# Kernel optimization log

Hardware: AMD Instinct MI355X
Metric: run time of the kernel (lower is better)

Reference implementation:

```python
import jax, jax.numpy as jnp
import numpy as np

EPS = 1e-8

def _cosine(a, b):
    # a: (b,h,s,d), b: (b,1,1,d) -> (b,h,s). torch eps semantics: clamp each norm.
    num = jnp.sum(a * b, axis=-1)
    na = jnp.maximum(jnp.linalg.norm(a, axis=-1), EPS)
    nb = jnp.maximum(jnp.linalg.norm(b, axis=-1), EPS)
    return num / (na * nb)

def setup_inputs() -> dict:
    B, H, S, DH, DM = 2, 16, 2048, 64, 1024
    key = jax.random.key(0)
    ks = jax.random.split(key, 8)
    queries = jax.random.normal(ks[0], (B, H, S, DH), dtype=jnp.float32)
    keys = jax.random.normal(ks[1], (B, H, S, DH), dtype=jnp.float32)
    context = jax.random.normal(ks[2], (B, DM), dtype=jnp.float32)
    prev_state = jax.random.normal(ks[3], (B, S, DH), dtype=jnp.float32)
    # causal mask (1 = keep, 0 = masked), shape (B,1,S,S)
    attention_mask = jnp.broadcast_to(jnp.tril(jnp.ones((S, S), dtype=jnp.int32)), (B, 1, S, S))
    # learned params (Linear weights stored torch-style as (out, in))
    cfm_ctx_w = jax.random.normal(ks[4], (DH, DM), dtype=jnp.float32) / np.sqrt(DM)
    cfm_state_w = jax.random.normal(ks[5], (DH, DH), dtype=jnp.float32) / np.sqrt(DH)
    afm_ctx_w = jax.random.normal(ks[6], (DH, DM), dtype=jnp.float32) / np.sqrt(DM)
    cfm_scale = jnp.full((1,), 0.1, dtype=jnp.float32)
    afm_scale = jnp.full((1,), 0.1, dtype=jnp.float32)
    alpha = jnp.asarray(0.1, dtype=jnp.float32)
    beta = jnp.asarray(0.1, dtype=jnp.float32)
    return dict(queries=queries, keys=keys, context=context, prev_state=prev_state,
                attention_mask=attention_mask, cfm_ctx_w=cfm_ctx_w, cfm_state_w=cfm_state_w,
                cfm_scale=cfm_scale, afm_ctx_w=afm_ctx_w, afm_scale=afm_scale,
                alpha=alpha, beta=beta)

def reference(queries, keys, context, prev_state, attention_mask,
              cfm_ctx_w, cfm_state_w, cfm_scale, afm_ctx_w, afm_scale, alpha, beta):
    B, H, S, DH = queries.shape
    # QK^T / sqrt(d_k): (b,h,s,s)
    attn_scores = jnp.einsum('bhqd,bhkd->bhqk', queries, keys) / jnp.sqrt(jnp.asarray(DH, queries.dtype))
    # ---- CFM ----
    cfm_ctx = (context @ cfm_ctx_w.T)[:, None, None, :]            # (b,1,1,dh)
    witt = _cosine(keys, cfm_ctx)                                   # (b,h,s)
    state = (prev_state @ cfm_state_w.T)[:, None, :, :]             # (b,1,s,dh)
    hamming = jnp.mean(((keys > 0) != (state > 0)).astype(keys.dtype), axis=-1)  # (b,h,s)
    cfm = ((witt + (1.0 - hamming)) * cfm_scale[0])[:, :, None, :]  # (b,h,1,s)
    # ---- AFM (no key_probs -> uniform entropy 1/S) ----
    afm_ctx = (context @ afm_ctx_w.T)[:, None, None, :]
    contradiction = jax.nn.relu(-_cosine(keys, afm_ctx))            # (b,h,s)
    entropy = jnp.full_like(contradiction, 1.0 / S)
    afm = ((contradiction + entropy) * afm_scale[0])[:, :, None, :]
    composite = attn_scores + alpha * cfm - beta * afm
    composite = jnp.where(attention_mask == 0, -jnp.inf, composite)
    return composite
```

## Files before the change

### kernel.cpp

```cpp
#include <hip/hip_runtime.h>
#include <math.h>

#define BB 2
#define HH 16
#define SS 2048
#define DHD 64
#define DMD 1024
#define EPSF 1e-8f
#define NEG_FILL -1.0e30f

typedef __attribute__((ext_vector_type(8))) short bf16x8;
typedef __attribute__((ext_vector_type(4))) float f32x4;

#define WS_BIAS_F   1024
#define WS_CONV_F   66560
#define CONV_ELEMS  (BB * HH * SS * DHD)
#define GRAN_TOTAL  (CONV_ELEMS / 8)
#define WS_NEEDED_B ((size_t)WS_CONV_F * 4 + (size_t)CONV_ELEMS * 2 * 4)

static __device__ __forceinline__ unsigned short f2bf(float f) {
    unsigned u = __float_as_uint(f);
    u += 0x7FFFu + ((u >> 16) & 1u);
    return (unsigned short)(u >> 16);
}
static __device__ __forceinline__ float bf2f(unsigned short h) {
    return __uint_as_float(((unsigned)h) << 16);
}
static __device__ __forceinline__ void cvt8(const float* p, bf16x8& h8, bf16x8& l8) {
    float4 v0 = *(const float4*)p;
    float4 v1 = *(const float4*)(p + 4);
    float vf[8] = {v0.x, v0.y, v0.z, v0.w, v1.x, v1.y, v1.z, v1.w};
    #pragma unroll
    for (int j = 0; j < 8; ++j) {
        unsigned short h = f2bf(vf[j]);
        h8[j] = (short)h;
        l8[j] = (short)f2bf(vf[j] - bf2f(h));
    }
}

__global__ void ctx_kernel(const float* __restrict__ context,
                           const float* __restrict__ cfm_ctx_w,
                           const float* __restrict__ afm_ctx_w,
                           float* __restrict__ ws) {
    int t = threadIdx.x;
    int b = t >> 7, sel = (t >> 6) & 1, o = t & 63;
    const float* W = sel ? afm_ctx_w : cfm_ctx_w;
    const float4* wrow = (const float4*)(W + o * DMD);
    const float4* crow = (const float4*)(context + b * DMD);
    float acc = 0.f;
    for (int m = 0; m < DMD / 4; ++m) {
        float4 w4 = wrow[m];
        float4 c4 = crow[m];
        acc += w4.x * c4.x + w4.y * c4.y + w4.z * c4.z + w4.w * c4.w;
    }
    ws[b * 128 + sel * 64 + o] = acc;
    float sq = acc * acc;
    for (int off = 32; off >= 1; off >>= 1) sq += __shfl_xor(sq, off);
    if (o == 0) ws[256 + b * 2 + sel] = fmaxf(sqrtf(sq), EPSF);
}

__global__ void bias_kernel(const float* __restrict__ keys,
                            const float* __restrict__ prev_state,
                            const float* __restrict__ cfm_state_w,
                            const float* __restrict__ cfm_scale,
                            const float* __restrict__ afm_scale,
                            const float* __restrict__ alpha_p,
                            const float* __restrict__ beta_p,
                            const float* __restrict__ ws_ctx,
                            float* __restrict__ bias_out) {
    int gid = blockIdx.x * 4 + (threadIdx.x >> 6);
    int b = gid >> 11, s = gid & (SS - 1);
    int l = threadIdx.x & 63;
    const float4* prow = (const float4*)(prev_state + ((size_t)b * SS + s) * DHD);
    const float4* wrow = (const float4*)(cfm_state_w + l * DHD);
    float st = 0.f;
    #pragma unroll
    for (int j = 0; j < DHD / 4; ++j) {
        float4 p4 = prow[j], w4 = wrow[j];
        st += p4.x * w4.x + p4.y * w4.y + p4.z * w4.z + p4.w * w4.w;
    }
    unsigned long long smask = __ballot(st > 0.f);

    int h = l >> 2, q = l & 3, d0 = q * 16;
    int sb = (int)((smask >> d0) & 0xFFFFull);
    const float* krow = keys + (((size_t)(b * HH + h)) * SS + s) * DHD + d0;
    const float* cc = ws_ctx + b * 128 + d0;
    const float* ac = ws_ctx + b * 128 + 64 + d0;
    float v0 = 0.f, v1 = 0.f, v2 = 0.f, mism = 0.f;
    #pragma unroll
    for (int j4 = 0; j4 < 4; ++j4) {
        float4 k4 = *(const float4*)(krow + j4 * 4);
        float4 c4 = *(const float4*)(cc + j4 * 4);
        float4 a4 = *(const float4*)(ac + j4 * 4);
        float kf[4] = {k4.x, k4.y, k4.z, k4.w};
        float cf[4] = {c4.x, c4.y, c4.z, c4.w};
        float af[4] = {a4.x, a4.y, a4.z, a4.w};
        #pragma unroll
        for (int j = 0; j < 4; ++j) {
            float kd = kf[j];
            v0 = fmaf(kd, cf[j], v0);
            v1 = fmaf(kd, af[j], v1);
            v2 = fmaf(kd, kd, v2);
            int bit = (sb >> (j4 * 4 + j)) & 1;
            mism += ((kd > 0.f) != (bit != 0)) ? 1.f : 0.f;
        }
    }
    v0 += __shfl_xor(v0, 1); v0 += __shfl_xor(v0, 2);
    v1 += __shfl_xor(v1, 1); v1 += __shfl_xor(v1, 2);
    v2 += __shfl_xor(v2, 1); v2 += __shfl_xor(v2, 2);
    mism += __shfl_xor(mism, 1); mism += __shfl_xor(mism, 2);
    if (q == 0) {
        float nb_c = ws_ctx[256 + b * 2];
        float nb_a = ws_ctx[256 + b * 2 + 1];
        float al = alpha_p[0] * cfm_scale[0];
        float be = beta_p[0] * afm_scale[0];
        float nk = fmaxf(sqrtf(v2), EPSF);
        float witt = v0 / (nk * nb_c);
        float contra = fmaxf(-(v1 / (nk * nb_a)), 0.f);
        float ham = mism * (1.f / 64.f);
        bias_out[(size_t)(b * HH + h) * SS + s] =
            al * (witt + 1.f - ham) - be * (contra + 1.f / (float)SS);
    }
}

__global__ void conv_kernel(const float* __restrict__ Q,
                            const float* __restrict__ K,
                            unsigned short* __restrict__ wsc) {
    int sel = blockIdx.y;
    const float* src = sel ? K : Q;
    float scale = sel ? 1.f : 0.125f;
    unsigned short* hi = wsc + (size_t)(sel ? 2 : 0) * CONV_ELEMS;
    unsigned short* lo = hi + CONV_ELEMS;
    int gid = blockIdx.x * 256 + threadIdx.x;
    int bh = gid >> 14;
    int rem = gid & 16383;
    int u = rem >> 7, r2 = rem & 127;
    int s = r2 >> 6, r3 = r2 & 63;
    int lg = r3 >> 4, lr = r3 & 15;
    size_t sidx = ((size_t)bh * SS + u * 16 + lr) * DHD + s * 32 + lg * 8;
    float4 a = *(const float4*)(src + sidx);
    float4 b = *(const float4*)(src + sidx + 4);
    float vf[8] = {a.x, a.y, a.z, a.w, b.x, b.y, b.z, b.w};
    bf16x8 h8, l8;
    #pragma unroll
    for (int j = 0; j < 8; ++j) {
        float f = vf[j] * scale;
        unsigned short h = f2bf(f);
        h8[j] = (short)h;
        l8[j] = (short)f2bf(f - bf2f(h));
    }
    *(bf16x8*)(hi + (size_t)gid * 8) = h8;
    *(bf16x8*)(lo + (size_t)gid * 8) = l8;
}

#define MFMA16(A, B, C) __builtin_amdgcn_mfma_f32_16x16x32_bf16(A, B, C, 0, 0, 0)

__global__ __launch_bounds__(256, 2) void band_pc(
    const unsigned short* __restrict__ wsc,
    const float* __restrict__ bias, float* __restrict__ out) {
    int L = blockIdx.x;
    int xcd = L & 7, sL = L >> 3;
    int j = sL & 31;
    int bh = ((sL >> 5) << 3) | xcd;
    int tid = threadIdx.x;
    int w = tid >> 6, l = tid & 63, lr = l & 15, lg = l >> 4;
    int lg4 = lg * 4;

    int chunksA = (j >> 1) + 1;
    int chunksA4 = (chunksA + 3) & ~3;
    int chunksZ = 32 - (j >> 1);
    int chunksZ4 = (chunksZ + 3) & ~3;
    if (chunksZ4 > 32) chunksZ4 = 32;
    int nchunks = chunksZ4;
    int ngroups = nchunks >> 2;
    int mygroupsA = chunksA4 >> 2;
    int fillA = chunksA4 * 64;
    int fillZ = chunksZ4 * 64;
    int rowA = j * 32, rowZ = (63 - j) * 32;
    int fr0 = 4 * (ngroups - mygroupsA);
    if (fr0 > 32) fr0 = 32;

    __shared__ unsigned short KB[2][8192];
    __shared__ float BIASL[2048];
    __shared__ float TR[2][16 * 256];

    const unsigned short* Qh = wsc;
    const unsigned short* Ql = Qh + CONV_ELEMS;
    const unsigned short* Kh = Ql + CONV_ELEMS;
    const unsigned short* Kl = Kh + CONV_ELEMS;
    const float* bias_g = bias + (size_t)bh * SS;
    float* ob = out + (size_t)bh * SS * SS;
    size_t kbase = (size_t)bh * 131072;
    f32x4 fneg = {NEG_FILL, NEG_FILL, NEG_FILL, NEG_FILL};

#define LOADCH(cidx, R) do {                                                 \
    _Pragma("unroll")                                                        \
    for (int gi = 0; gi < 8; ++gi) {                                         \
        int g = pw * 8 + gi, u = g >> 2, q = g & 3;                          \
        const unsigned short* src = (q < 2 ? Kh : Kl) + kbase                \
            + (size_t)((cidx) * 4 + u) * 1024 + (q & 1) * 512 + l * 8;       \
        R[gi] = *(const bf16x8*)src;                                         \
    }                                                                        \
} while (0)

#define WRITECH(R, nb) do {                                                  \
    _Pragma("unroll")                                                        \
    for (int gi = 0; gi < 8; ++gi) {                                         \
        int g = pw * 8 + gi, u = g >> 2, q = g & 3;                          \
        *(bf16x8*)&KB[nb][u * 2048 + q * 512 + l * 8] = R[gi];               \
    }                                                                        \
} while (0)

    if (w >= 2) {
        int pw = w - 2;
        #pragma unroll
        for (int i = 0; i < 4; ++i) {
            f32x4 bv = *(const f32x4*)(bias_g + pw * 1024 + i * 256 + l * 4);
            *(f32x4*)&BIASL[pw * 1024 + i * 256 + l * 4] = bv;
        }
        bf16x8 rE[8], rO[8];
        LOADCH(0, rE);
        LOADCH(1, rO);
        WRITECH(rE, 0);
        asm volatile("s_waitcnt lgkmcnt(0)" ::: "memory");
        __builtin_amdgcn_sched_barrier(0);
        for (int c = 0; c < nchunks; c += 2) {
            __builtin_amdgcn_s_barrier();
            if (c + 1 < nchunks) WRITECH(rO, 1);
            if (c + 2 < nchunks) LOADCH(c + 2, rE);
            asm volatile("s_waitcnt lgkmcnt(0)" ::: "memory");
            __builtin_amdgcn_sched_barrier(0);
            __builtin_amdgcn_s_barrier();
            if (c + 2 < nchunks) WRITECH(rE, 0);
            if (c + 3 < nchunks) LOADCH(c + 3, rO);
            asm volatile("s_waitcnt lgkmcnt(0)" ::: "memory");
            __builtin_amdgcn_sched_barrier(0);
        }
    } else {
        int row0 = (w == 0) ? rowA : rowZ;
        int mygroups = (w == 0) ? mygroupsA : ngroups;
        float* trw = &TR[w][0];
        int fr = 0;
        bf16x8 q0h0, q0h1, q0l0, q0l1, q1h0, q1h1, q1l0, q1l1;
        {
            size_t qb = kbase + (size_t)(row0 >> 4) * 1024;
            q0h0 = *(const bf16x8*)(Qh + qb + l * 8);
            q0h1 = *(const bf16x8*)(Qh + qb + 512 + l * 8);
            q1h0 = *(const bf16x8*)(Qh + qb + 1024 + l * 8);
            q1h1 = *(const bf16x8*)(Qh + qb + 1536 + l * 8);
            q0l0 = *(const bf16x8*)(Ql + qb + l * 8);
            q0l1 = *(const bf16x8*)(Ql + qb + 512 + l * 8);
            q1l0 = *(const bf16x8*)(Ql + qb + 1024 + l * 8);
            q1l1 = *(const bf16x8*)(Ql + qb + 1536 + l * 8);
        }
        f32x4 acc0[16], acc1[16];
        for (int g = 0; g < ngroups; ++g) {
            if (g < mygroups) {
                #pragma unroll
                for (int cc = 0; cc < 4; ++cc) {
                    __builtin_amdgcn_s_barrier();
                    const unsigned short* kb = &KB[cc & 1][0];
                    #pragma unroll
                    for (int u = 0; u < 4; ++u) {
                        int ui = cc * 4 + u;
                        int ug = g * 16 + ui;
                        bf16x8 kh0 = *(const bf16x8*)&kb[u * 2048 + l * 8];
                        bf16x8 kh1 = *(const bf16x8*)&kb[u * 2048 + 512 + l * 8];
                        bf16x8 kl0 = *(const bf16x8*)&kb[u * 2048 + 1024 + l * 8];
                        bf16x8 kl1 = *(const bf16x8*)&kb[u * 2048 + 1536 + l * 8];
                        f32x4 bv = *(const f32x4*)&BIASL[ug * 16 + lg4];
                        int c0 = ug * 16 + lg4;
                        {
                            int row = row0 + lr;
                            f32x4 a = {0.f, 0.f, 0.f, 0.f};
                            a = MFMA16(kh0, q0h0, a);
                            a = MFMA16(kh1, q0h1, a);
                            a = MFMA16(kh0, q0l0, a);
                            a = MFMA16(kh1, q0l1, a);
                            a = MFMA16(kl0, q0h0, a);
                            a = MFMA16(kl1, q0h1, a);
                            #pragma unroll
                            for (int e = 0; e < 4; ++e) {
                                float x = a[e] + bv[e];
                                if (c0 + e > row) x = NEG_FILL;
                                a[e] = x;
                            }
                            acc0[ui] = a;
                        }
                        {
                            int row = row0 + 16 + lr;
                            f32x4 a = {0.f, 0.f, 0.f, 0.f};
                            a = MFMA16(kh0, q1h0, a);
                            a = MFMA16(kh1, q1h1, a);
                            a = MFMA16(kh0, q1l0, a);
                            a = MFMA16(kh1, q1l1, a);
                            a = MFMA16(kl0, q1h0, a);
                            a = MFMA16(kl1, q1h1, a);
                            #pragma unroll
                            for (int e = 0; e < 4; ++e) {
                                float x = a[e] + bv[e];
                                if (c0 + e > row) x = NEG_FILL;
                                a[e] = x;
                            }
                            acc1[ui] = a;
                        }
                    }
                }
                #pragma unroll
                for (int u16 = 0; u16 < 16; ++u16)
                    *(f32x4*)&trw[lr * 256 + ((u16 * 16 + lg4) ^ ((lr & 7) << 2))] = acc0[u16];
                asm volatile("s_waitcnt lgkmcnt(0)" ::: "memory");
                __builtin_amdgcn_sched_barrier(0);
                #pragma unroll
                for (int r = 0; r < 16; ++r) {
                    f32x4 v = *(const f32x4*)&trw[r * 256 + ((l * 4) ^ ((r & 7) << 2))];
                    __builtin_nontemporal_store(v,
                        (f32x4*)(ob + (size_t)(row0 + r) * SS + g * 256 + l * 4));
                }
                asm volatile("s_waitcnt lgkmcnt(0)" ::: "memory");
                __builtin_amdgcn_sched_barrier(0);
                #pragma unroll
                for (int u16 = 0; u16 < 16; ++u16)
                    *(f32x4*)&trw[lr * 256 + ((u16 * 16 + lg4) ^ ((lr & 7) << 2))] = acc1[u16];
                asm volatile("s_waitcnt lgkmcnt(0)" ::: "memory");
                __builtin_amdgcn_sched_barrier(0);
                #pragma unroll
                for (int r = 0; r < 16; ++r) {
                    f32x4 v = *(const f32x4*)&trw[r * 256 + ((l * 4) ^ ((r & 7) << 2))];
                    __builtin_nontemporal_store(v,
                        (f32x4*)(ob + (size_t)(row0 + 16 + r) * SS + g * 256 + l * 4));
                }
                asm volatile("s_waitcnt lgkmcnt(0)" ::: "memory");
                __builtin_amdgcn_sched_barrier(0);
            } else {
                #pragma unroll
                for (int cc = 0; cc < 4; ++cc) {
                    __builtin_amdgcn_s_barrier();
                    if (fr < 32) {
                        float* orow = ob + (size_t)(rowA + fr) * SS;
                        for (int c = fillA + l * 4; c < SS; c += 256)
                            __builtin_nontemporal_store(fneg, (f32x4*)(orow + c));
                        ++fr;
                    }
                }
            }
        }
    }

    {
        int remA = 32 - fr0;
        int nZ = (fillZ < SS) ? 32 : 0;
        int total = remA + nZ;
        for (int i = w; i < total; i += 4) {
            int row, f0;
            if (i < remA) { row = rowA + fr0 + i; f0 = fillA; }
            else          { row = rowZ + (i - remA); f0 = fillZ; }
            float* orow = ob + (size_t)row * SS;
            for (int c = f0 + l * 4; c < SS; c += 256)
                __builtin_nontemporal_store(fneg, (f32x4*)(orow + c));
        }
    }
#undef LOADCH
#undef WRITECH
}

#define LOADB(S, unit) do {                                                  \
    size_t _r = ((size_t)bh * SS + (unit) * 16 + lr) * DHD + lg * 8;         \
    cvt8(K + _r, S##h0, S##l0);                                              \
    cvt8(K + _r + 32, S##h1, S##l1);                                         \
    S##bv = *(const f32x4*)(bias_row + (unit) * 16 + lg4);                   \
} while (0)

#define COMP(S, unit) do {                                                   \
    int _c0 = (unit) * 16 + lg4;                                             \
    {                                                                        \
        int _row = row0 + lr;                                                \
        f32x4 _a = {0.f, 0.f, 0.f, 0.f};                                     \
        _a = MFMA16(S##h0, q0h0, _a);                                        \
        _a = MFMA16(S##h1, q0h1, _a);                                        \
        _a = MFMA16(S##h0, q0l0, _a);                                        \
        _a = MFMA16(S##h1, q0l1, _a);                                        \
        _a = MFMA16(S##l0, q0h0, _a);                                        \
        _a = MFMA16(S##l1, q0h1, _a);                                        \
        f32x4 _v;                                                            \
        _Pragma("unroll")                                                    \
        for (int _e = 0; _e < 4; ++_e) {                                     \
            float _x = fmaf(_a[_e], 0.125f, S##bv[_e]);                      \
            if (_c0 + _e > _row) _x = NEG_FILL;                              \
            _v[_e] = _x;                                                     \
        }                                                                    \
        __builtin_nontemporal_store(_v, (f32x4*)(ob + (size_t)_row * SS + _c0)); \
    }                                                                        \
    {                                                                        \
        int _row = row0 + 16 + lr;                                           \
        f32x4 _a = {0.f, 0.f, 0.f, 0.f};                                     \
        _a = MFMA16(S##h0, q1h0, _a);                                        \
        _a = MFMA16(S##h1, q1h1, _a);                                        \
        _a = MFMA16(S##h0, q1l0, _a);                                        \
        _a = MFMA16(S##h1, q1l1, _a);                                        \
        _a = MFMA16(S##l0, q1h0, _a);                                        \
        _a = MFMA16(S##l1, q1h1, _a);                                        \
        f32x4 _v;                                                            \
        _Pragma("unroll")                                                    \
        for (int _e = 0; _e < 4; ++_e) {                                     \
            float _x = fmaf(_a[_e], 0.125f, S##bv[_e]);                      \
            if (_c0 + _e > _row) _x = NEG_FILL;                              \
            _v[_e] = _x;                                                     \
        }                                                                    \
        __builtin_nontemporal_store(_v, (f32x4*)(ob + (size_t)_row * SS + _c0)); \
    }                                                                        \
} while (0)

__global__ __launch_bounds__(128, 2) void band_fallback(
    const float* __restrict__ Q, const float* __restrict__ K,
    const float* __restrict__ bias, float* __restrict__ out) {
    int L = blockIdx.x;
    int xcd = L & 7, sL = L >> 3;
    int j = sL & 31;
    int bh = ((sL >> 5) << 3) | xcd;
    int tid = threadIdx.x;
    int w = tid >> 6, l = tid & 63, lr = l & 15, lg = l >> 4;
    int lg4 = lg * 4;
    int band = w ? (63 - j) : j;
    int row0 = band * 32;
    int nunits = 2 * band + 2;

    const float* bias_row = bias + (size_t)bh * SS;
    float* ob = out + (size_t)bh * SS * SS;

    bf16x8 q0h0, q0h1, q0l0, q0l1, q1h0, q1h1, q1l0, q1l1;
    {
        size_t qr0 = ((size_t)bh * SS + row0 + lr) * DHD + lg * 8;
        cvt8(Q + qr0, q0h0, q0l0);
        cvt8(Q + qr0 + 32, q0h1, q0l1);
        size_t qr1 = qr0 + (size_t)16 * DHD;
        cvt8(Q + qr1, q1h0, q1l0);
        cvt8(Q + qr1 + 32, q1h1, q1l1);
    }

    bf16x8 Ah0, Ah1, Al0, Al1, Bh0, Bh1, Bl0, Bl1;
    f32x4 Abv, Bbv;
    LOADB(A, 0);
    LOADB(B, 1);
    for (int u = 0; u < nunits; u += 2) {
        COMP(A, u);
        if (u + 2 < nunits) LOADB(A, u + 2);
        COMP(B, u + 1);
        if (u + 3 < nunits) LOADB(B, u + 3);
    }

    f32x4 f4 = {NEG_FILL, NEG_FILL, NEG_FILL, NEG_FILL};
    int fill0 = nunits * 16;
    for (int r = 0; r < 32; ++r) {
        float* orow = ob + (size_t)(row0 + r) * SS;
        for (int c = fill0 + l * 4; c < SS; c += 256)
            __builtin_nontemporal_store(f4, (f32x4*)(orow + c));
    }
}

extern "C" void kernel_launch(void* const* d_in, const int* in_sizes, int n_in,
                              void* d_out, int out_size, void* d_ws, size_t ws_size,
                              hipStream_t stream) {
    const float* queries     = (const float*)d_in[0];
    const float* keys        = (const float*)d_in[1];
    const float* context     = (const float*)d_in[2];
    const float* prev_state  = (const float*)d_in[3];
    const float* cfm_ctx_w   = (const float*)d_in[5];
    const float* cfm_state_w = (const float*)d_in[6];
    const float* cfm_scale   = (const float*)d_in[7];
    const float* afm_ctx_w   = (const float*)d_in[8];
    const float* afm_scale   = (const float*)d_in[9];
    const float* alpha_p     = (const float*)d_in[10];
    const float* beta_p      = (const float*)d_in[11];
    float* out = (float*)d_out;
    float* ws  = (float*)d_ws;
    float* bias = ws + WS_BIAS_F;
    unsigned short* wsc = (unsigned short*)(ws + WS_CONV_F);

    ctx_kernel<<<1, 256, 0, stream>>>(context, cfm_ctx_w, afm_ctx_w, ws);
    bias_kernel<<<BB * SS / 4, 256, 0, stream>>>(keys, prev_state, cfm_state_w,
                                                 cfm_scale, afm_scale, alpha_p,
                                                 beta_p, ws, bias);
    if (ws_size >= WS_NEEDED_B) {
        conv_kernel<<<dim3(GRAN_TOTAL / 256, 2), 256, 0, stream>>>(
            queries, keys, wsc);
        band_pc<<<1024, 256, 0, stream>>>(wsc, bias, out);
    } else {
        band_fallback<<<1024, 128, 0, stream>>>(queries, keys, bias, out);
    }
}
```

Before: 195.2 us.

## Convert Q inline in band kernel, pre-convert only K, drop LDS waits

The pre-conversion kernel now splits only K into bf16 hi/lo pairs. Each band block instead loads its own Q rows as fp32 and converts them in registers, with the 1/8 scale folded in, which halves the conversion traffic and workspace. The fallback path also folds the scale into Q, so its epilogue becomes a plain add rather than an fma. Two explicit LDS waitcnt/sched_barrier pairs in the transpose-store epilogue are removed, which lets the compiler overlap that work but relies on its own dependency tracking for correctness.

```diff
diff --git a/kernel.cpp b/kernel.cpp
--- a/kernel.cpp
+++ b/kernel.cpp
@@ -16,7 +16,7 @@
 #define WS_CONV_F   66560
 #define CONV_ELEMS  (BB * HH * SS * DHD)
 #define GRAN_TOTAL  (CONV_ELEMS / 8)
-#define WS_NEEDED_B ((size_t)WS_CONV_F * 4 + (size_t)CONV_ELEMS * 2 * 4)
+#define WS_NEEDED_B ((size_t)WS_CONV_F * 4 + (size_t)CONV_ELEMS * 2 * 2)
 
 static __device__ __forceinline__ unsigned short f2bf(float f) {
     unsigned u = __float_as_uint(f);
@@ -26,15 +26,17 @@
 static __device__ __forceinline__ float bf2f(unsigned short h) {
     return __uint_as_float(((unsigned)h) << 16);
 }
-static __device__ __forceinline__ void cvt8(const float* p, bf16x8& h8, bf16x8& l8) {
+static __device__ __forceinline__ void cvt8s(const float* p, float scale,
+                                             bf16x8& h8, bf16x8& l8) {
     float4 v0 = *(const float4*)p;
     float4 v1 = *(const float4*)(p + 4);
     float vf[8] = {v0.x, v0.y, v0.z, v0.w, v1.x, v1.y, v1.z, v1.w};
     #pragma unroll
     for (int j = 0; j < 8; ++j) {
-        unsigned short h = f2bf(vf[j]);
+        float f = vf[j] * scale;
+        unsigned short h = f2bf(f);
         h8[j] = (short)h;
-        l8[j] = (short)f2bf(vf[j] - bf2f(h));
+        l8[j] = (short)f2bf(f - bf2f(h));
     }
 }
 
@@ -123,14 +125,10 @@
     }
 }
 
-__global__ void conv_kernel(const float* __restrict__ Q,
-                            const float* __restrict__ K,
+__global__ void conv_kernel(const float* __restrict__ K,
                             unsigned short* __restrict__ wsc) {
-    int sel = blockIdx.y;
-    const float* src = sel ? K : Q;
-    float scale = sel ? 1.f : 0.125f;
-    unsigned short* hi = wsc + (size_t)(sel ? 2 : 0) * CONV_ELEMS;
-    unsigned short* lo = hi + CONV_ELEMS;
+    unsigned short* hi = wsc;
+    unsigned short* lo = wsc + CONV_ELEMS;
     int gid = blockIdx.x * 256 + threadIdx.x;
     int bh = gid >> 14;
     int rem = gid & 16383;
@@ -138,17 +136,8 @@
     int s = r2 >> 6, r3 = r2 & 63;
     int lg = r3 >> 4, lr = r3 & 15;
     size_t sidx = ((size_t)bh * SS + u * 16 + lr) * DHD + s * 32 + lg * 8;
-    float4 a = *(const float4*)(src + sidx);
-    float4 b = *(const float4*)(src + sidx + 4);
-    float vf[8] = {a.x, a.y, a.z, a.w, b.x, b.y, b.z, b.w};
     bf16x8 h8, l8;
-    #pragma unroll
-    for (int j = 0; j < 8; ++j) {
-        float f = vf[j] * scale;
-        unsigned short h = f2bf(f);
-        h8[j] = (short)h;
-        l8[j] = (short)f2bf(f - bf2f(h));
-    }
+    cvt8s(K + sidx, 1.f, h8, l8);
     *(bf16x8*)(hi + (size_t)gid * 8) = h8;
     *(bf16x8*)(lo + (size_t)gid * 8) = l8;
 }
@@ -156,6 +145,7 @@
 #define MFMA16(A, B, C) __builtin_amdgcn_mfma_f32_16x16x32_bf16(A, B, C, 0, 0, 0)
 
 __global__ __launch_bounds__(256, 2) void band_pc(
+    const float* __restrict__ Qf,
     const unsigned short* __restrict__ wsc,
     const float* __restrict__ bias, float* __restrict__ out) {
     int L = blockIdx.x;
@@ -184,10 +174,8 @@
     __shared__ float BIASL[2048];
     __shared__ float TR[2][16 * 256];
 
-    const unsigned short* Qh = wsc;
-    const unsigned short* Ql = Qh + CONV_ELEMS;
-    const unsigned short* Kh = Ql + CONV_ELEMS;
-    const unsigned short* Kl = Kh + CONV_ELEMS;
+    const unsigned short* Kh = wsc;
+    const unsigned short* Kl = wsc + CONV_ELEMS;
     const float* bias_g = bias + (size_t)bh * SS;
     float* ob = out + (size_t)bh * SS * SS;
     size_t kbase = (size_t)bh * 131072;
@@ -243,15 +231,11 @@
         int fr = 0;
         bf16x8 q0h0, q0h1, q0l0, q0l1, q1h0, q1h1, q1l0, q1l1;
         {
-            size_t qb = kbase + (size_t)(row0 >> 4) * 1024;
-            q0h0 = *(const bf16x8*)(Qh + qb + l * 8);
-            q0h1 = *(const bf16x8*)(Qh + qb + 512 + l * 8);
-            q1h0 = *(const bf16x8*)(Qh + qb + 1024 + l * 8);
-            q1h1 = *(const bf16x8*)(Qh + qb + 1536 + l * 8);
-            q0l0 = *(const bf16x8*)(Ql + qb + l * 8);
-            q0l1 = *(const bf16x8*)(Ql + qb + 512 + l * 8);
-            q1l0 = *(const bf16x8*)(Ql + qb + 1024 + l * 8);
-            q1l1 = *(const bf16x8*)(Ql + qb + 1536 + l * 8);
+            const float* qp = Qf + ((size_t)bh * SS + row0 + lr) * DHD + lg * 8;
+            cvt8s(qp, 0.125f, q0h0, q0l0);
+            cvt8s(qp + 32, 0.125f, q0h1, q0l1);
+            cvt8s(qp + (size_t)16 * DHD, 0.125f, q1h0, q1l0);
+            cvt8s(qp + (size_t)16 * DHD + 32, 0.125f, q1h1, q1l1);
         }
         f32x4 acc0[16], acc1[16];
         for (int g = 0; g < ngroups; ++g) {
@@ -317,8 +301,6 @@
                     __builtin_nontemporal_store(v,
                         (f32x4*)(ob + (size_t)(row0 + r) * SS + g * 256 + l * 4));
                 }
-                asm volatile("s_waitcnt lgkmcnt(0)" ::: "memory");
-                __builtin_amdgcn_sched_barrier(0);
                 #pragma unroll
                 for (int u16 = 0; u16 < 16; ++u16)
                     *(f32x4*)&trw[lr * 256 + ((u16 * 16 + lg4) ^ ((lr & 7) << 2))] = acc1[u16];
@@ -330,8 +312,6 @@
                     __builtin_nontemporal_store(v,
                         (f32x4*)(ob + (size_t)(row0 + 16 + r) * SS + g * 256 + l * 4));
                 }
-                asm volatile("s_waitcnt lgkmcnt(0)" ::: "memory");
-                __builtin_amdgcn_sched_barrier(0);
             } else {
                 #pragma unroll
                 for (int cc = 0; cc < 4; ++cc) {
@@ -366,8 +346,8 @@
 
 #define LOADB(S, unit) do {                                                  \
     size_t _r = ((size_t)bh * SS + (unit) * 16 + lr) * DHD + lg * 8;         \
-    cvt8(K + _r, S##h0, S##l0);                                              \
-    cvt8(K + _r + 32, S##h1, S##l1);                                         \
+    cvt8s(K + _r, 1.f, S##h0, S##l0);                                        \
+    cvt8s(K + _r + 32, 1.f, S##h1, S##l1);                                   \
     S##bv = *(const f32x4*)(bias_row + (unit) * 16 + lg4);                   \
 } while (0)
 
@@ -385,7 +365,7 @@
         f32x4 _v;                                                            \
         _Pragma("unroll")                                                    \
         for (int _e = 0; _e < 4; ++_e) {                                     \
-            float _x = fmaf(_a[_e], 0.125f, S##bv[_e]);                      \
+            float _x = _a[_e] + S##bv[_e];                                   \
             if (_c0 + _e > _row) _x = NEG_FILL;                              \
             _v[_e] = _x;                                                     \
         }                                                                    \
@@ -403,7 +383,7 @@
         f32x4 _v;                                                            \
         _Pragma("unroll")                                                    \
         for (int _e = 0; _e < 4; ++_e) {                                     \
-            float _x = fmaf(_a[_e], 0.125f, S##bv[_e]);                      \
+            float _x = _a[_e] + S##bv[_e];                                   \
             if (_c0 + _e > _row) _x = NEG_FILL;                              \
             _v[_e] = _x;                                                     \
         }                                                                    \
@@ -430,12 +410,11 @@
 
     bf16x8 q0h0, q0h1, q0l0, q0l1, q1h0, q1h1, q1l0, q1l1;
     {
-        size_t qr0 = ((size_t)bh * SS + row0 + lr) * DHD + lg * 8;
-        cvt8(Q + qr0, q0h0, q0l0);
-        cvt8(Q + qr0 + 32, q0h1, q0l1);
-        size_t qr1 = qr0 + (size_t)16 * DHD;
-        cvt8(Q + qr1, q1h0, q1l0);
-        cvt8(Q + qr1 + 32, q1h1, q1l1);
+        const float* qp = Q + ((size_t)bh * SS + row0 + lr) * DHD + lg * 8;
+        cvt8s(qp, 0.125f, q0h0, q0l0);
+        cvt8s(qp + 32, 0.125f, q0h1, q0l1);
+        cvt8s(qp + (size_t)16 * DHD, 0.125f, q1h0, q1l0);
+        cvt8s(qp + (size_t)16 * DHD + 32, 0.125f, q1h1, q1l1);
     }
 
     bf16x8 Ah0, Ah1, Al0, Al1, Bh0, Bh1, Bl0, Bl1;
@@ -482,9 +461,8 @@
                                                  cfm_scale, afm_scale, alpha_p,
                                                  beta_p, ws, bias);
     if (ws_size >= WS_NEEDED_B) {
-        conv_kernel<<<dim3(GRAN_TOTAL / 256, 2), 256, 0, stream>>>(
-            queries, keys, wsc);
-        band_pc<<<1024, 256, 0, stream>>>(wsc, bias, out);
+        conv_kernel<<<GRAN_TOTAL / 256, 256, 0, stream>>>(keys, wsc);
+        band_pc<<<1024, 256, 0, stream>>>(queries, wsc, bias, out);
     } else {
         band_fallback<<<1024, 128, 0, stream>>>(queries, keys, bias, out);
     }
```

Result: no change. 192.3 us (median of 2 runs) (-1.5%).
